# Optimization experiments

Measured on AMD Instinct MI355X. Metric: run time of the kernel, lower is better.

The kernel has to match this reference:

```python
import jax, jax.numpy as jnp
import numpy as np
import math

N_EMBD = 1024
N_HEAD = 16
HEAD_DIM = N_EMBD // N_HEAD

def setup_inputs() -> dict:
    key = jax.random.key(0)
    ks = jax.random.split(key, 9)
    B, T, C = 2, 2048, N_EMBD
    s = 1.0 / math.sqrt(C)
    return {
        "x": jax.random.normal(ks[0], (B, T, C), dtype=jnp.float32),
        "Wq": jax.random.normal(ks[1], (C, C), dtype=jnp.float32) * s,
        "bq": jnp.zeros((C,), dtype=jnp.float32),
        "Wk": jax.random.normal(ks[2], (C, C), dtype=jnp.float32) * s,
        "bk": jnp.zeros((C,), dtype=jnp.float32),
        "Wv": jax.random.normal(ks[3], (C, C), dtype=jnp.float32) * s,
        "bv": jnp.zeros((C,), dtype=jnp.float32),
        "Wp": jax.random.normal(ks[4], (C, C), dtype=jnp.float32) * s,
        "bp": jnp.zeros((C,), dtype=jnp.float32),
    }

def reference(x, Wq, bq, Wk, bk, Wv, bv, Wp, bp):
    B, T, C = x.shape
    H, D = N_HEAD, HEAD_DIM
    q = (x @ Wq + bq).reshape(B, T, H, D).transpose(0, 2, 1, 3)  # [B,H,T,D]
    k = (x @ Wk + bk).reshape(B, T, H, D).transpose(0, 2, 1, 3)
    v = (x @ Wv + bv).reshape(B, T, H, D).transpose(0, 2, 1, 3)
    att = jnp.einsum('bhqd,bhkd->bhqk', q, k) / math.sqrt(D)
    causal = jnp.tril(jnp.ones((T, T), dtype=bool))
    att = jnp.where(causal, att, -jnp.inf)
    att = jax.nn.softmax(att, axis=-1)
    att = jnp.nan_to_num(att)
    y = jnp.einsum('bhqk,bhkd->bhqd', att, v)
    y = y.transpose(0, 2, 1, 3).reshape(B, T, C)
    return y @ Wp + bp
```

## Files before the change

### kernel.cpp

```cpp
#include <hip/hip_runtime.h>
#include <hip/hip_bf16.h>
#include <stdint.h>

typedef unsigned short u16;
typedef __attribute__((ext_vector_type(8))) short short8;
typedef __attribute__((ext_vector_type(4))) float f32x4;

static __device__ __forceinline__ u16 f2bf(float f) {
  unsigned u = __builtin_bit_cast(unsigned, f);
  u += 0x7fffu + ((u >> 16) & 1u);
  return (u16)(u >> 16);
}

static __device__ __forceinline__ unsigned cvtpk(float lo, float hi) {
  unsigned r;
  asm("v_cvt_pk_bf16_f32 %0, %1, %2" : "=v"(r) : "v"(lo), "v"(hi));
  return r;
}

static __device__ __forceinline__ void gload16(const u16* g, u16* l) {
  __builtin_amdgcn_global_load_lds(
      (__attribute__((address_space(1))) void*)const_cast<u16*>(g),
      (__attribute__((address_space(3))) void*)l, 16, 0, 0);
}

__global__ __launch_bounds__(256) void prep_kernel(
    const float* __restrict__ x, const float* __restrict__ Wq,
    const float* __restrict__ Wk, const float* __restrict__ Wv,
    const float* __restrict__ Wp, u16* __restrict__ xb, u16* __restrict__ wt) {
  __shared__ float tile[64][65];
  int b = blockIdx.x;
  if (b < 2048) {
    size_t i = (size_t)b * 256 + threadIdx.x;
    const float4* xp = (const float4*)x + i * 2;
    float4 a = xp[0], v = xp[1];
    union { u16 u[8]; int4 q; } r;
    r.u[0] = f2bf(a.x); r.u[1] = f2bf(a.y); r.u[2] = f2bf(a.z); r.u[3] = f2bf(a.w);
    r.u[4] = f2bf(v.x); r.u[5] = f2bf(v.y); r.u[6] = f2bf(v.z); r.u[7] = f2bf(v.w);
    *(int4*)(xb + i * 8) = r.q;
  } else {
    int wb = b - 2048;
    int wz = wb >> 8, r8 = wb & 255;
    const float* W = (wz == 0) ? Wq : (wz == 1) ? Wk : (wz == 2) ? Wv : Wp;
    int n0 = (r8 & 15) * 64, k0 = (r8 >> 4) * 64;
    int tx = threadIdx.x & 63, ty = threadIdx.x >> 6;
#pragma unroll
    for (int r = 0; r < 16; ++r)
      tile[ty + 4 * r][tx] = W[(size_t)(k0 + ty + 4 * r) * 1024 + n0 + tx];
    __syncthreads();
    u16* dst = wt + (size_t)wz * 1024 * 1024;
#pragma unroll
    for (int r = 0; r < 16; ++r) {
      int n = ty + 4 * r;
      dst[(size_t)(n0 + n) * 1024 + k0 + tx] = f2bf(tile[tx][n]);
    }
  }
}

__global__ __launch_bounds__(256, 2) void gemm_qkv_kernel(
    const u16* __restrict__ A, const u16* __restrict__ Bt, int Kdim,
    int GM, int GN, int RM, int RN,
    u16* __restrict__ qd, u16* __restrict__ kd, u16* __restrict__ vd,
    const float* __restrict__ bq, const float* __restrict__ bk,
    const float* __restrict__ bv) {
  __shared__ u16 Alds[8192];
  __shared__ u16 Blds[8192];
  int tid = threadIdx.x;
  int lane = tid & 63, w = tid >> 6;
  int l15 = lane & 15, lg = lane >> 4;
  int flat = blockIdx.x;
  int xcd = flat & 7, idx = flat >> 3;
  int rnc = GN / RN;
  int rm = (xcd / rnc) * RM, rn = (xcd % rnc) * RN;
  int im = idx % RM, in_ = idx / RM;
  int m0 = (rm + im) * 128, n0 = (rn + in_) * 128;
  int wm = (w >> 1) * 64, wn = (w & 1) * 64;
  int srow = lane >> 3;
  int colsw = ((lane & 7) * 8) ^ ((srow & 7) * 8);

  const u16* pA[4];
  const u16* pB[4];
  int dls[4];
#pragma unroll
  for (int j = 0; j < 4; ++j) {
    int issue = w * 4 + j;
    int row = issue * 8 + srow;
    pA[j] = A + (size_t)(m0 + row) * Kdim + colsw;
    pB[j] = Bt + (size_t)(n0 + row) * Kdim + colsw;
    dls[j] = issue * 512;
  }
  int kx = (l15 & 7) << 4;
  int ofs0 = (lg * 16) ^ kx, ofs1 = (64 + lg * 16) ^ kx;
  int rbA = (wm + l15) * 128, rbB = (wn + l15) * 128;

  f32x4 acc[4][4] = {};
  for (int kt = 0; kt < Kdim; kt += 64) {
#pragma unroll
    for (int j = 0; j < 4; ++j) {
      gload16(pA[j], Alds + dls[j]);
      gload16(pB[j], Blds + dls[j]);
      pA[j] += 64; pB[j] += 64;
    }
    __syncthreads();
    __builtin_amdgcn_s_setprio(1);
#pragma unroll
    for (int kk = 0; kk < 2; ++kk) {
      int o_ = kk ? ofs1 : ofs0;
      short8 a[4], b[4];
#pragma unroll
      for (int mt = 0; mt < 4; ++mt)
        a[mt] = *(const short8*)((const char*)Alds + (rbA + o_) + mt * 2048);
#pragma unroll
      for (int nt = 0; nt < 4; ++nt)
        b[nt] = *(const short8*)((const char*)Blds + (rbB + o_) + nt * 2048);
#pragma unroll
      for (int mt = 0; mt < 4; ++mt)
#pragma unroll
        for (int nt = 0; nt < 4; ++nt)
          acc[mt][nt] = __builtin_amdgcn_mfma_f32_16x16x32_bf16(a[mt], b[nt],
                                                                acc[mt][nt], 0, 0, 0);
    }
    __builtin_amdgcn_s_setprio(0);
    __syncthreads();
  }
#pragma unroll
  for (int nt = 0; nt < 4; ++nt) {
    int n = n0 + wn + nt * 16 + l15;
    int wi = n >> 10, nn = n & 1023, h = nn >> 6, d = nn & 63;
    const float* bb = (wi == 0) ? bq : (wi == 1) ? bk : bv;
    float bval = bb[nn];
    if (wi == 2) {
#pragma unroll
      for (int mt = 0; mt < 4; ++mt) {
        int m = m0 + wm + mt * 16 + lg * 4;
        int mb = m >> 11, t = m & 2047;
        unsigned lo = cvtpk(acc[mt][nt][0] + bval, acc[mt][nt][1] + bval);
        unsigned hi = cvtpk(acc[mt][nt][2] + bval, acc[mt][nt][3] + bval);
        *(uint2*)&vd[((size_t)(mb * 16 + h) * 64 + d) * 2048 + t] =
            make_uint2(lo, hi);
      }
    } else {
      u16* dst = (wi == 0) ? qd : kd;
#pragma unroll
      for (int mt = 0; mt < 4; ++mt) {
#pragma unroll
        for (int i = 0; i < 4; ++i) {
          int m = m0 + wm + mt * 16 + lg * 4 + i;
          int mb = m >> 11, t = m & 2047;
          dst[((size_t)(mb * 16 + h) * 2048 + t) * 64 + d] =
              f2bf(acc[mt][nt][i] + bval);
        }
      }
    }
  }
}

__global__ __launch_bounds__(256, 2) void gemm_proj_kernel(
    const u16* __restrict__ A, const u16* __restrict__ Bt,
    float* __restrict__ outf, const float* __restrict__ bias1) {
  __shared__ u16 Alds[2 * 8192];
  __shared__ u16 Blds[2 * 4096];
  int tid = threadIdx.x;
  int lane = tid & 63, w = tid >> 6;
  int l15 = lane & 15, lg = lane >> 4;
  int flat = blockIdx.x;
  int xcd = flat & 7, idx = flat >> 3;
  int rm = (xcd >> 1) * 8, rn = (xcd & 1) * 8;
  int m0 = (rm + (idx & 7)) * 128, n0 = (rn + (idx >> 3)) * 64;
  int wm = (w >> 1) * 64, wn = (w & 1) * 32;
  int srow = lane >> 3;
  int colsw = ((lane & 7) * 8) ^ ((srow & 7) * 8);

  const u16* pA[4];
  int dlsA[4];
#pragma unroll
  for (int j = 0; j < 4; ++j) {
    int issue = w * 4 + j;
    int row = issue * 8 + srow;
    pA[j] = A + (size_t)(m0 + row) * 1024 + colsw;
    dlsA[j] = issue * 512;
  }
  const u16* pB[2];
  int dlsB[2];
#pragma unroll
  for (int it = 0; it < 2; ++it) {
    int chunk = it * 256 + tid;
    int row = chunk >> 3;
    int col = ((chunk & 7) * 8) ^ ((row & 7) * 8);
    pB[it] = Bt + (size_t)(n0 + row) * 1024 + col;
    dlsB[it] = (it * 256 + w * 64) * 8;
  }
  int kx = (l15 & 7) << 4;
  int ofs0 = (lg * 16) ^ kx, ofs1 = (64 + lg * 16) ^ kx;
  int rbA = (wm + l15) * 128, rbB = (wn + l15) * 128;

  auto stage = [&](int buf) {
    u16* Ad = Alds + buf * 8192;
    u16* Bd = Blds + buf * 4096;
#pragma unroll
    for (int j = 0; j < 4; ++j) { gload16(pA[j], Ad + dlsA[j]); pA[j] += 64; }
#pragma unroll
    for (int it = 0; it < 2; ++it) { gload16(pB[it], Bd + dlsB[it]); pB[it] += 64; }
  };

  f32x4 acc[4][2] = {};
  stage(0);
  int cur = 0;
  for (int kt = 0; kt < 1024; kt += 64) {
    __syncthreads();
    if (kt + 64 < 1024) stage(cur ^ 1);
    const char* Al = (const char*)Alds + cur * 16384;
    const char* Bl = (const char*)Blds + cur * 8192;
    __builtin_amdgcn_s_setprio(1);
#pragma unroll
    for (int kk = 0; kk < 2; ++kk) {
      int o_ = kk ? ofs1 : ofs0;
      short8 a[4], b[2];
#pragma unroll
      for (int mt = 0; mt < 4; ++mt)
        a[mt] = *(const short8*)(Al + (rbA + o_) + mt * 2048);
#pragma unroll
      for (int nt = 0; nt < 2; ++nt)
        b[nt] = *(const short8*)(Bl + (rbB + o_) + nt * 2048);
#pragma unroll
      for (int mt = 0; mt < 4; ++mt)
#pragma unroll
        for (int nt = 0; nt < 2; ++nt)
          acc[mt][nt] = __builtin_amdgcn_mfma_f32_16x16x32_bf16(a[mt], b[nt],
                                                                acc[mt][nt], 0, 0, 0);
    }
    __builtin_amdgcn_s_setprio(0);
    cur ^= 1;
  }
#pragma unroll
  for (int nt = 0; nt < 2; ++nt) {
    int n = n0 + wn + nt * 16 + l15;
    float bval = bias1[n];
#pragma unroll
    for (int mt = 0; mt < 4; ++mt) {
#pragma unroll
      for (int i = 0; i < 4; ++i) {
        int m = m0 + wm + mt * 16 + lg * 4 + i;
        outf[(size_t)m * 1024 + n] = acc[mt][nt][i] + bval;
      }
    }
  }
}

__global__ __launch_bounds__(256, 4) void fattn_kernel(const u16* __restrict__ qb,
                                                       const u16* __restrict__ kb,
                                                       const u16* __restrict__ vt,
                                                       u16* __restrict__ y) {
  __shared__ u16 Klds[4096];
  __shared__ u16 Vlds[4096];
  __shared__ u16 Plds[4096];
  int tid = threadIdx.x, lane = tid & 63, w = tid >> 6;
  int l15 = lane & 15, lg = lane >> 4;
  int flat = blockIdx.x;
  int bh = flat & 31;
  int g = flat >> 5;
  int qt;
  switch (g >> 3) {
    case 0:  qt = 31 - g; break;
    case 1:  qt = g - 8;  break;
    case 2:  qt = 39 - g; break;
    default: qt = g - 16; break;
  }
  size_t base = (size_t)bh * 2048 * 64;
  int mb = bh >> 4, h = bh & 15;
  const float SC = 0.125f * 1.44269504088896340736f;
  const float NINF = -__builtin_inff();

  int r0 = tid >> 3, c0 = ((tid & 7) * 8) ^ ((r0 & 7) << 3);
  int r1 = (256 + tid) >> 3, c1 = ((tid & 7) * 8) ^ ((r1 & 7) << 3);
  const u16* pK0 = kb + base + (size_t)r0 * 64 + c0;
  const u16* pK1 = kb + base + (size_t)r1 * 64 + c1;
  const u16* pV0 = vt + base + (size_t)r0 * 2048 + c0;
  const u16* pV1 = vt + base + (size_t)r1 * 2048 + c1;
  int dk0 = w * 512, dk1 = (256 + w * 64) * 8;
  int kx = (l15 & 7) << 4;
  int rb0 = l15 * 128 + ((lg * 16) ^ kx);
  int rb1 = l15 * 128 + ((64 + lg * 16) ^ kx);
  char* pbase = (char*)Plds + w * 2048;
  int pw0 = l15 * 128 + ((lg * 8) ^ kx);
  int pw1 = l15 * 128 + ((32 + lg * 8) ^ kx);
  int pw2 = l15 * 128 + ((64 + lg * 8) ^ kx);
  int pw3 = l15 * 128 + ((96 + lg * 8) ^ kx);

  int qw = qt * 64 + w * 16;
  int qr = qw + l15;
  short8 qf[2];
#pragma unroll
  for (int kk = 0; kk < 2; ++kk)
    qf[kk] = *(const short8*)&qb[base + (size_t)qr * 64 + kk * 32 + lg * 8];
  f32x4 o[4] = {};
  float mrow = NINF, lrow = 0.f;
  int ntiles = qt + 1;
  for (int j = 0; j < ntiles; ++j) {
    gload16(pK0, Klds + dk0); gload16(pK1, Klds + dk1);
    gload16(pV0, Vlds + dk0); gload16(pV1, Vlds + dk1);
    pK0 += 4096; pK1 += 4096; pV0 += 64; pV1 += 64;
    __syncthreads();
    f32x4 s[4] = {};
    __builtin_amdgcn_s_setprio(1);
#pragma unroll
    for (int kk = 0; kk < 2; ++kk) {
      int o_ = kk ? rb1 : rb0;
      short8 ka[4];
#pragma unroll
      for (int nt = 0; nt < 4; ++nt)
        ka[nt] = *(const short8*)((const char*)Klds + o_ + nt * 2048);
#pragma unroll
      for (int nt = 0; nt < 4; ++nt)
        s[nt] = __builtin_amdgcn_mfma_f32_16x16x32_bf16(ka[nt], qf[kk], s[nt], 0, 0, 0);
    }
    __builtin_amdgcn_s_setprio(0);
    float rs[16];
    if (j == qt) {
      int k0 = j * 64;
#pragma unroll
      for (int nt = 0; nt < 4; ++nt)
#pragma unroll
        for (int i = 0; i < 4; ++i) {
          int ka_ = k0 + nt * 16 + lg * 4 + i;
          rs[nt * 4 + i] = (ka_ > qr) ? NINF : s[nt][i];
        }
    } else {
#pragma unroll
      for (int nt = 0; nt < 4; ++nt)
#pragma unroll
        for (int i = 0; i < 4; ++i) rs[nt * 4 + i] = s[nt][i];
    }
    float rmax = fmaxf(
        fmaxf(fmaxf(fmaxf(rs[0], rs[1]), fmaxf(rs[2], rs[3])),
              fmaxf(fmaxf(rs[4], rs[5]), fmaxf(rs[6], rs[7]))),
        fmaxf(fmaxf(fmaxf(rs[8], rs[9]), fmaxf(rs[10], rs[11])),
              fmaxf(fmaxf(rs[12], rs[13]), fmaxf(rs[14], rs[15]))));
    float tmax = rmax * SC;
    if (!__all(tmax <= mrow + 8.f)) {
      float t2 = fmaxf(tmax, __shfl_xor(tmax, 16));
      t2 = fmaxf(t2, __shfl_xor(t2, 32));
      float vmax = fmaxf(t2, mrow);
      float scale = exp2f(mrow - vmax);
      mrow = vmax;
      lrow *= scale;
#pragma unroll
      for (int dn = 0; dn < 4; ++dn) o[dn] *= scale;
    }
    float p[16];
#pragma unroll
    for (int u = 0; u < 16; ++u) p[u] = exp2f(fmaf(rs[u], SC, -mrow));
    float pr0 = ((p[0] + p[1]) + (p[2] + p[3])) + ((p[4] + p[5]) + (p[6] + p[7]));
    float pr1 = ((p[8] + p[9]) + (p[10] + p[11])) + ((p[12] + p[13]) + (p[14] + p[15]));
    lrow += pr0 + pr1;
    *(uint2*)(pbase + pw0) = make_uint2(cvtpk(p[0], p[1]), cvtpk(p[2], p[3]));
    *(uint2*)(pbase + pw1) = make_uint2(cvtpk(p[4], p[5]), cvtpk(p[6], p[7]));
    *(uint2*)(pbase + pw2) = make_uint2(cvtpk(p[8], p[9]), cvtpk(p[10], p[11]));
    *(uint2*)(pbase + pw3) = make_uint2(cvtpk(p[12], p[13]), cvtpk(p[14], p[15]));
    __builtin_amdgcn_s_setprio(1);
#pragma unroll
    for (int kk = 0; kk < 2; ++kk) {
      int o_ = kk ? rb1 : rb0;
      short8 ap = *(const short8*)(pbase + o_);
#pragma unroll
      for (int dn = 0; dn < 4; ++dn) {
        short8 bv_ = *(const short8*)((const char*)Vlds + o_ + dn * 2048);
        o[dn] = __builtin_amdgcn_mfma_f32_16x16x32_bf16(bv_, ap, o[dn], 0, 0, 0);
      }
    }
    __builtin_amdgcn_s_setprio(0);
    __syncthreads();
  }
  lrow += __shfl_xor(lrow, 16);
  lrow += __shfl_xor(lrow, 32);
  float inv = 1.f / lrow;
  size_t rb = ((size_t)(mb * 2048 + qr)) * 1024 + (size_t)h * 64;
#pragma unroll
  for (int dn = 0; dn < 4; ++dn) {
    unsigned lo = cvtpk(o[dn][0] * inv, o[dn][1] * inv);
    unsigned hi = cvtpk(o[dn][2] * inv, o[dn][3] * inv);
    *(uint2*)&y[rb + dn * 16 + lg * 4] = make_uint2(lo, hi);
  }
}

extern "C" void kernel_launch(void* const* d_in, const int* in_sizes, int n_in,
                              void* d_out, int out_size, void* d_ws, size_t ws_size,
                              hipStream_t stream) {
  const float* x  = (const float*)d_in[0];
  const float* Wq = (const float*)d_in[1];
  const float* bq = (const float*)d_in[2];
  const float* Wk = (const float*)d_in[3];
  const float* bk = (const float*)d_in[4];
  const float* Wv = (const float*)d_in[5];
  const float* bv = (const float*)d_in[6];
  const float* Wp = (const float*)d_in[7];
  const float* bp = (const float*)d_in[8];
  float* out = (float*)d_out;
  char* ws = (char*)d_ws;
  u16* xb   = (u16*)(ws);
  u16* wt   = (u16*)(ws + ((size_t)8 << 20));
  u16* qbuf = (u16*)(ws + ((size_t)16 << 20));
  u16* kbuf = (u16*)(ws + ((size_t)24 << 20));
  u16* vtb  = (u16*)(ws + ((size_t)32 << 20));
  u16* ybuf = (u16*)(ws + ((size_t)40 << 20));

  prep_kernel<<<dim3(3072), dim3(256), 0, stream>>>(x, Wq, Wk, Wv, Wp, xb, wt);
  gemm_qkv_kernel<<<dim3(768), dim3(256), 0, stream>>>(
      xb, wt, 1024, 32, 24, 8, 12, qbuf, kbuf, vtb, bq, bk, bv);
  fattn_kernel<<<dim3(1024), dim3(256), 0, stream>>>(qbuf, kbuf, vtb, ybuf);
  gemm_proj_kernel<<<dim3(512), dim3(256), 0, stream>>>(
      ybuf, wt + (size_t)3 * 1024 * 1024, out, bp);
  (void)in_sizes; (void)n_in; (void)out_size; (void)ws_size;
}
```

Before: 101.5 us.

## Split causal attention KV range into paired halves and merge with combine kernel

Each attention block now processes two partial query tiles: the first half of the KV range for tile u and the second half for tile 31-u. This evens out the causal-triangle work per block, which previously ranged from 1 to 32 KV tiles. Each half writes unnormalized bf16 output plus its per-row (max, sum) statistics. A new combine kernel then rescales and merges the two halves into the final y. The cost is an extra kernel launch, extra global traffic for the partial outputs and statistics, and an extra bf16 rounding of the partial outputs. The partial buffers reuse workspace regions whose earlier contents (x and the Q/K/V weights) have already been consumed.

```diff
diff --git a/kernel.cpp b/kernel.cpp
--- a/kernel.cpp
+++ b/kernel.cpp
@@ -10,6 +10,11 @@
   unsigned u = __builtin_bit_cast(unsigned, f);
   u += 0x7fffu + ((u >> 16) & 1u);
   return (u16)(u >> 16);
+}
+
+static __device__ __forceinline__ float bf2f(u16 v) {
+  unsigned u = (unsigned)v << 16;
+  return __builtin_bit_cast(float, u);
 }
 
 static __device__ __forceinline__ unsigned cvtpk(float lo, float hi) {
@@ -247,10 +252,10 @@
   }
 }
 
-__global__ __launch_bounds__(256, 4) void fattn_kernel(const u16* __restrict__ qb,
-                                                       const u16* __restrict__ kb,
-                                                       const u16* __restrict__ vt,
-                                                       u16* __restrict__ y) {
+__global__ __launch_bounds__(256, 4) void fattn_kernel(
+    const u16* __restrict__ qb, const u16* __restrict__ kb,
+    const u16* __restrict__ vt, u16* __restrict__ y,
+    u16* __restrict__ poA, float2* __restrict__ mlA, float2* __restrict__ mlB) {
   __shared__ u16 Klds[4096];
   __shared__ u16 Vlds[4096];
   __shared__ u16 Plds[4096];
@@ -258,14 +263,7 @@
   int l15 = lane & 15, lg = lane >> 4;
   int flat = blockIdx.x;
   int bh = flat & 31;
-  int g = flat >> 5;
-  int qt;
-  switch (g >> 3) {
-    case 0:  qt = 31 - g; break;
-    case 1:  qt = g - 8;  break;
-    case 2:  qt = 39 - g; break;
-    default: qt = g - 16; break;
-  }
+  int u = flat >> 5;
   size_t base = (size_t)bh * 2048 * 64;
   int mb = bh >> 4, h = bh & 15;
   const float SC = 0.125f * 1.44269504088896340736f;
@@ -273,10 +271,6 @@
 
   int r0 = tid >> 3, c0 = ((tid & 7) * 8) ^ ((r0 & 7) << 3);
   int r1 = (256 + tid) >> 3, c1 = ((tid & 7) * 8) ^ ((r1 & 7) << 3);
-  const u16* pK0 = kb + base + (size_t)r0 * 64 + c0;
-  const u16* pK1 = kb + base + (size_t)r1 * 64 + c1;
-  const u16* pV0 = vt + base + (size_t)r0 * 2048 + c0;
-  const u16* pV1 = vt + base + (size_t)r1 * 2048 + c1;
   int dk0 = w * 512, dk1 = (256 + w * 64) * 8;
   int kx = (l15 & 7) << 4;
   int rb0 = l15 * 128 + ((lg * 16) ^ kx);
@@ -287,100 +281,136 @@
   int pw2 = l15 * 128 + ((64 + lg * 8) ^ kx);
   int pw3 = l15 * 128 + ((96 + lg * 8) ^ kx);
 
-  int qw = qt * 64 + w * 16;
-  int qr = qw + l15;
-  short8 qf[2];
-#pragma unroll
-  for (int kk = 0; kk < 2; ++kk)
-    qf[kk] = *(const short8*)&qb[base + (size_t)qr * 64 + kk * 32 + lg * 8];
-  f32x4 o[4] = {};
-  float mrow = NINF, lrow = 0.f;
-  int ntiles = qt + 1;
-  for (int j = 0; j < ntiles; ++j) {
-    gload16(pK0, Klds + dk0); gload16(pK1, Klds + dk1);
-    gload16(pV0, Vlds + dk0); gload16(pV1, Vlds + dk1);
-    pK0 += 4096; pK1 += 4096; pV0 += 64; pV1 += 64;
-    __syncthreads();
-    f32x4 s[4] = {};
-    __builtin_amdgcn_s_setprio(1);
-#pragma unroll
-    for (int kk = 0; kk < 2; ++kk) {
-      int o_ = kk ? rb1 : rb0;
-      short8 ka[4];
-#pragma unroll
-      for (int nt = 0; nt < 4; ++nt)
-        ka[nt] = *(const short8*)((const char*)Klds + o_ + nt * 2048);
-#pragma unroll
-      for (int nt = 0; nt < 4; ++nt)
-        s[nt] = __builtin_amdgcn_mfma_f32_16x16x32_bf16(ka[nt], qf[kk], s[nt], 0, 0, 0);
-    }
-    __builtin_amdgcn_s_setprio(0);
-    float rs[16];
-    if (j == qt) {
-      int k0 = j * 64;
-#pragma unroll
-      for (int nt = 0; nt < 4; ++nt)
-#pragma unroll
-        for (int i = 0; i < 4; ++i) {
-          int ka_ = k0 + nt * 16 + lg * 4 + i;
-          rs[nt * 4 + i] = (ka_ > qr) ? NINF : s[nt][i];
+  for (int pc = 0; pc < 2; ++pc) {
+    int qt = pc ? (31 - u) : u;
+    int sp = (qt + 2) >> 1;
+    int j0 = pc ? sp : 0;
+    int j1 = pc ? (qt + 1) : sp;
+    int qw = qt * 64 + w * 16;
+    int qr = qw + l15;
+    short8 qf[2];
+#pragma unroll
+    for (int kk = 0; kk < 2; ++kk)
+      qf[kk] = *(const short8*)&qb[base + (size_t)qr * 64 + kk * 32 + lg * 8];
+    f32x4 o[4] = {};
+    float mrow = NINF, lrow = 0.f;
+    const u16* pK0 = kb + base + (size_t)(j0 * 64 + r0) * 64 + c0;
+    const u16* pK1 = kb + base + (size_t)(j0 * 64 + r1) * 64 + c1;
+    const u16* pV0 = vt + base + (size_t)r0 * 2048 + j0 * 64 + c0;
+    const u16* pV1 = vt + base + (size_t)r1 * 2048 + j0 * 64 + c1;
+    for (int j = j0; j < j1; ++j) {
+      gload16(pK0, Klds + dk0); gload16(pK1, Klds + dk1);
+      gload16(pV0, Vlds + dk0); gload16(pV1, Vlds + dk1);
+      pK0 += 4096; pK1 += 4096; pV0 += 64; pV1 += 64;
+      __syncthreads();
+      f32x4 s[4] = {};
+      __builtin_amdgcn_s_setprio(1);
+#pragma unroll
+      for (int kk = 0; kk < 2; ++kk) {
+        int o_ = kk ? rb1 : rb0;
+        short8 ka[4];
+#pragma unroll
+        for (int nt = 0; nt < 4; ++nt)
+          ka[nt] = *(const short8*)((const char*)Klds + o_ + nt * 2048);
+#pragma unroll
+        for (int nt = 0; nt < 4; ++nt)
+          s[nt] = __builtin_amdgcn_mfma_f32_16x16x32_bf16(ka[nt], qf[kk], s[nt], 0, 0, 0);
+      }
+      __builtin_amdgcn_s_setprio(0);
+      float rs[16];
+      if (j == qt) {
+        int k0 = j * 64;
+#pragma unroll
+        for (int nt = 0; nt < 4; ++nt)
+#pragma unroll
+          for (int i = 0; i < 4; ++i) {
+            int ka_ = k0 + nt * 16 + lg * 4 + i;
+            rs[nt * 4 + i] = (ka_ > qr) ? NINF : s[nt][i];
+          }
+      } else {
+#pragma unroll
+        for (int nt = 0; nt < 4; ++nt)
+#pragma unroll
+          for (int i = 0; i < 4; ++i) rs[nt * 4 + i] = s[nt][i];
+      }
+      float rmax = fmaxf(
+          fmaxf(fmaxf(fmaxf(rs[0], rs[1]), fmaxf(rs[2], rs[3])),
+                fmaxf(fmaxf(rs[4], rs[5]), fmaxf(rs[6], rs[7]))),
+          fmaxf(fmaxf(fmaxf(rs[8], rs[9]), fmaxf(rs[10], rs[11])),
+                fmaxf(fmaxf(rs[12], rs[13]), fmaxf(rs[14], rs[15]))));
+      float tmax = rmax * SC;
+      if (!__all(tmax <= mrow + 8.f)) {
+        float t2 = fmaxf(tmax, __shfl_xor(tmax, 16));
+        t2 = fmaxf(t2, __shfl_xor(t2, 32));
+        float vmax = fmaxf(t2, mrow);
+        float scale = exp2f(mrow - vmax);
+        mrow = vmax;
+        lrow *= scale;
+#pragma unroll
+        for (int dn = 0; dn < 4; ++dn) o[dn] *= scale;
+      }
+      float p[16];
+#pragma unroll
+      for (int u2 = 0; u2 < 16; ++u2) p[u2] = exp2f(fmaf(rs[u2], SC, -mrow));
+      float pr0 = ((p[0] + p[1]) + (p[2] + p[3])) + ((p[4] + p[5]) + (p[6] + p[7]));
+      float pr1 = ((p[8] + p[9]) + (p[10] + p[11])) + ((p[12] + p[13]) + (p[14] + p[15]));
+      lrow += pr0 + pr1;
+      *(uint2*)(pbase + pw0) = make_uint2(cvtpk(p[0], p[1]), cvtpk(p[2], p[3]));
+      *(uint2*)(pbase + pw1) = make_uint2(cvtpk(p[4], p[5]), cvtpk(p[6], p[7]));
+      *(uint2*)(pbase + pw2) = make_uint2(cvtpk(p[8], p[9]), cvtpk(p[10], p[11]));
+      *(uint2*)(pbase + pw3) = make_uint2(cvtpk(p[12], p[13]), cvtpk(p[14], p[15]));
+      __builtin_amdgcn_s_setprio(1);
+#pragma unroll
+      for (int kk = 0; kk < 2; ++kk) {
+        int o_ = kk ? rb1 : rb0;
+        short8 ap = *(const short8*)(pbase + o_);
+#pragma unroll
+        for (int dn = 0; dn < 4; ++dn) {
+          short8 bv_ = *(const short8*)((const char*)Vlds + o_ + dn * 2048);
+          o[dn] = __builtin_amdgcn_mfma_f32_16x16x32_bf16(bv_, ap, o[dn], 0, 0, 0);
         }
-    } else {
-#pragma unroll
-      for (int nt = 0; nt < 4; ++nt)
-#pragma unroll
-        for (int i = 0; i < 4; ++i) rs[nt * 4 + i] = s[nt][i];
-    }
-    float rmax = fmaxf(
-        fmaxf(fmaxf(fmaxf(rs[0], rs[1]), fmaxf(rs[2], rs[3])),
-              fmaxf(fmaxf(rs[4], rs[5]), fmaxf(rs[6], rs[7]))),
-        fmaxf(fmaxf(fmaxf(rs[8], rs[9]), fmaxf(rs[10], rs[11])),
-              fmaxf(fmaxf(rs[12], rs[13]), fmaxf(rs[14], rs[15]))));
-    float tmax = rmax * SC;
-    if (!__all(tmax <= mrow + 8.f)) {
-      float t2 = fmaxf(tmax, __shfl_xor(tmax, 16));
-      t2 = fmaxf(t2, __shfl_xor(t2, 32));
-      float vmax = fmaxf(t2, mrow);
-      float scale = exp2f(mrow - vmax);
-      mrow = vmax;
-      lrow *= scale;
-#pragma unroll
-      for (int dn = 0; dn < 4; ++dn) o[dn] *= scale;
-    }
-    float p[16];
-#pragma unroll
-    for (int u = 0; u < 16; ++u) p[u] = exp2f(fmaf(rs[u], SC, -mrow));
-    float pr0 = ((p[0] + p[1]) + (p[2] + p[3])) + ((p[4] + p[5]) + (p[6] + p[7]));
-    float pr1 = ((p[8] + p[9]) + (p[10] + p[11])) + ((p[12] + p[13]) + (p[14] + p[15]));
-    lrow += pr0 + pr1;
-    *(uint2*)(pbase + pw0) = make_uint2(cvtpk(p[0], p[1]), cvtpk(p[2], p[3]));
-    *(uint2*)(pbase + pw1) = make_uint2(cvtpk(p[4], p[5]), cvtpk(p[6], p[7]));
-    *(uint2*)(pbase + pw2) = make_uint2(cvtpk(p[8], p[9]), cvtpk(p[10], p[11]));
-    *(uint2*)(pbase + pw3) = make_uint2(cvtpk(p[12], p[13]), cvtpk(p[14], p[15]));
-    __builtin_amdgcn_s_setprio(1);
-#pragma unroll
-    for (int kk = 0; kk < 2; ++kk) {
-      int o_ = kk ? rb1 : rb0;
-      short8 ap = *(const short8*)(pbase + o_);
-#pragma unroll
-      for (int dn = 0; dn < 4; ++dn) {
-        short8 bv_ = *(const short8*)((const char*)Vlds + o_ + dn * 2048);
-        o[dn] = __builtin_amdgcn_mfma_f32_16x16x32_bf16(bv_, ap, o[dn], 0, 0, 0);
-      }
-    }
-    __builtin_amdgcn_s_setprio(0);
-    __syncthreads();
-  }
-  lrow += __shfl_xor(lrow, 16);
-  lrow += __shfl_xor(lrow, 32);
-  float inv = 1.f / lrow;
-  size_t rb = ((size_t)(mb * 2048 + qr)) * 1024 + (size_t)h * 64;
-#pragma unroll
-  for (int dn = 0; dn < 4; ++dn) {
-    unsigned lo = cvtpk(o[dn][0] * inv, o[dn][1] * inv);
-    unsigned hi = cvtpk(o[dn][2] * inv, o[dn][3] * inv);
-    *(uint2*)&y[rb + dn * 16 + lg * 4] = make_uint2(lo, hi);
-  }
+      }
+      __builtin_amdgcn_s_setprio(0);
+      __syncthreads();
+    }
+    lrow += __shfl_xor(lrow, 16);
+    lrow += __shfl_xor(lrow, 32);
+    size_t rb = ((size_t)(mb * 2048 + qr)) * 1024 + (size_t)h * 64;
+    u16* dst = pc ? y : poA;
+#pragma unroll
+    for (int dn = 0; dn < 4; ++dn) {
+      unsigned lo = cvtpk(o[dn][0], o[dn][1]);
+      unsigned hi = cvtpk(o[dn][2], o[dn][3]);
+      *(uint2*)&dst[rb + dn * 16 + lg * 4] = make_uint2(lo, hi);
+    }
+    if (lg == 0)
+      (pc ? mlB : mlA)[bh * 2048 + qr] = make_float2(mrow, lrow);
+  }
+}
+
+__global__ __launch_bounds__(256) void combine_kernel(
+    const u16* __restrict__ poA, const float2* __restrict__ mlA,
+    const float2* __restrict__ mlB, u16* __restrict__ y) {
+  int idx = blockIdx.x * 256 + threadIdx.x;
+  int pos = idx * 4;
+  int row = pos >> 10;
+  int hq = (pos >> 6) & 15;
+  int qr = row & 2047, mb2 = row >> 11;
+  int rid = (mb2 * 16 + hq) * 2048 + qr;
+  float2 a = mlA[rid], b = mlB[rid];
+  float m = fmaxf(a.x, b.x);
+  float ea = exp2f(a.x - m), eb = exp2f(b.x - m);
+  float inv = 1.f / (a.y * ea + b.y * eb);
+  ea *= inv; eb *= inv;
+  uint2 pa = *(const uint2*)&poA[pos];
+  uint2 pb = *(const uint2*)&y[pos];
+  const u16* au = (const u16*)&pa;
+  const u16* bu = (const u16*)&pb;
+  float v0 = bf2f(au[0]) * ea + bf2f(bu[0]) * eb;
+  float v1 = bf2f(au[1]) * ea + bf2f(bu[1]) * eb;
+  float v2 = bf2f(au[2]) * ea + bf2f(bu[2]) * eb;
+  float v3 = bf2f(au[3]) * ea + bf2f(bu[3]) * eb;
+  *(uint2*)&y[pos] = make_uint2(cvtpk(v0, v1), cvtpk(v2, v3));
 }
 
 extern "C" void kernel_launch(void* const* d_in, const int* in_sizes, int n_in,
@@ -403,11 +433,16 @@
   u16* kbuf = (u16*)(ws + ((size_t)24 << 20));
   u16* vtb  = (u16*)(ws + ((size_t)32 << 20));
   u16* ybuf = (u16*)(ws + ((size_t)40 << 20));
+  u16*    poA = (u16*)(ws);
+  float2* mlA = (float2*)(ws + ((size_t)8 << 20));
+  float2* mlB = (float2*)(ws + ((size_t)8 << 20) + (512 << 10));
 
   prep_kernel<<<dim3(3072), dim3(256), 0, stream>>>(x, Wq, Wk, Wv, Wp, xb, wt);
   gemm_qkv_kernel<<<dim3(768), dim3(256), 0, stream>>>(
       xb, wt, 1024, 32, 24, 8, 12, qbuf, kbuf, vtb, bq, bk, bv);
-  fattn_kernel<<<dim3(1024), dim3(256), 0, stream>>>(qbuf, kbuf, vtb, ybuf);
+  fattn_kernel<<<dim3(1024), dim3(256), 0, stream>>>(qbuf, kbuf, vtb, ybuf,
+                                                     poA, mlA, mlB);
+  combine_kernel<<<dim3(4096), dim3(256), 0, stream>>>(poA, mlA, mlB, ybuf);
   gemm_proj_kernel<<<dim3(512), dim3(256), 0, stream>>>(
       ybuf, wt + (size_t)3 * 1024 * 1024, out, bp);
   (void)in_sizes; (void)n_in; (void)out_size; (void)ws_size;
```

Result: slower. 110.4 us (+8.7%).

## Process 128-key K/V tiles per iteration in causal flash attention

Applied to the files above, without the earlier changes.

Doubles the K/V tile per loop iteration from 64 to 128 keys, doubling the K and V LDS buffers and updating the load addressing and swizzle for the wider V rows. This halves the number of barriers, global-to-LDS load rounds and online-softmax max/rescale checks per query tile. P·V is done in two 64-key halves that reuse the per-wave P buffer. The cost is more LDS per block, which could limit occupancy, plus wasted compute on a fully masked half tile at the diagonal when the query tile index is even.

```diff
diff --git a/kernel.cpp b/kernel.cpp
--- a/kernel.cpp
+++ b/kernel.cpp
@@ -251,8 +251,8 @@
                                                        const u16* __restrict__ kb,
                                                        const u16* __restrict__ vt,
                                                        u16* __restrict__ y) {
-  __shared__ u16 Klds[4096];
-  __shared__ u16 Vlds[4096];
+  __shared__ u16 Klds[8192];
+  __shared__ u16 Vlds[8192];
   __shared__ u16 Plds[4096];
   int tid = threadIdx.x, lane = tid & 63, w = tid >> 6;
   int l15 = lane & 15, lg = lane >> 4;
@@ -271,16 +271,22 @@
   const float SC = 0.125f * 1.44269504088896340736f;
   const float NINF = -__builtin_inff();
 
-  int r0 = tid >> 3, c0 = ((tid & 7) * 8) ^ ((r0 & 7) << 3);
-  int r1 = (256 + tid) >> 3, c1 = ((tid & 7) * 8) ^ ((r1 & 7) << 3);
-  const u16* pK0 = kb + base + (size_t)r0 * 64 + c0;
-  const u16* pK1 = kb + base + (size_t)r1 * 64 + c1;
-  const u16* pV0 = vt + base + (size_t)r0 * 2048 + c0;
-  const u16* pV1 = vt + base + (size_t)r1 * 2048 + c1;
-  int dk0 = w * 512, dk1 = (256 + w * 64) * 8;
+  const u16* pK[4];
+  const u16* pV[4];
+  int dls[4];
+#pragma unroll
+  for (int it = 0; it < 4; ++it) {
+    int c = it * 256 + tid;
+    int rK = c >> 3, cK = ((c & 7) * 8) ^ ((rK & 7) << 3);
+    pK[it] = kb + base + (size_t)rK * 64 + cK;
+    int dV = c >> 4, cV = ((c & 15) * 8) ^ ((dV & 7) << 3);
+    pV[it] = vt + base + (size_t)dV * 2048 + cV;
+    dls[it] = (it * 256 + w * 64) * 8;
+  }
   int kx = (l15 & 7) << 4;
-  int rb0 = l15 * 128 + ((lg * 16) ^ kx);
-  int rb1 = l15 * 128 + ((64 + lg * 16) ^ kx);
+  int ofs0 = (lg * 16) ^ kx, ofs1 = (64 + lg * 16) ^ kx;
+  int rb0 = l15 * 128 + ofs0, rb1 = l15 * 128 + ofs1;
+  int vb0 = l15 * 256 + ofs0, vb1 = l15 * 256 + ofs1;
   char* pbase = (char*)Plds + w * 2048;
   int pw0 = l15 * 128 + ((lg * 8) ^ kx);
   int pw1 = l15 * 128 + ((32 + lg * 8) ^ kx);
@@ -289,19 +295,23 @@
 
   int qw = qt * 64 + w * 16;
   int qr = qw + l15;
+  int jdiag = qt >> 1;
   short8 qf[2];
 #pragma unroll
   for (int kk = 0; kk < 2; ++kk)
     qf[kk] = *(const short8*)&qb[base + (size_t)qr * 64 + kk * 32 + lg * 8];
   f32x4 o[4] = {};
   float mrow = NINF, lrow = 0.f;
-  int ntiles = qt + 1;
-  for (int j = 0; j < ntiles; ++j) {
-    gload16(pK0, Klds + dk0); gload16(pK1, Klds + dk1);
-    gload16(pV0, Vlds + dk0); gload16(pV1, Vlds + dk1);
-    pK0 += 4096; pK1 += 4096; pV0 += 64; pV1 += 64;
-    __syncthreads();
-    f32x4 s[4] = {};
+  int ntiles = (qt + 2) >> 1;
+  for (int jj = 0; jj < ntiles; ++jj) {
+#pragma unroll
+    for (int it = 0; it < 4; ++it) {
+      gload16(pK[it], Klds + dls[it]);
+      gload16(pV[it], Vlds + dls[it]);
+      pK[it] += 8192; pV[it] += 128;
+    }
+    __syncthreads();
+    f32x4 s0[4] = {}, s1[4] = {};
     __builtin_amdgcn_s_setprio(1);
 #pragma unroll
     for (int kk = 0; kk < 2; ++kk) {
@@ -312,30 +322,48 @@
         ka[nt] = *(const short8*)((const char*)Klds + o_ + nt * 2048);
 #pragma unroll
       for (int nt = 0; nt < 4; ++nt)
-        s[nt] = __builtin_amdgcn_mfma_f32_16x16x32_bf16(ka[nt], qf[kk], s[nt], 0, 0, 0);
+        s0[nt] = __builtin_amdgcn_mfma_f32_16x16x32_bf16(ka[nt], qf[kk], s0[nt], 0, 0, 0);
+    }
+#pragma unroll
+    for (int kk = 0; kk < 2; ++kk) {
+      int o_ = 8192 + (kk ? rb1 : rb0);
+      short8 ka[4];
+#pragma unroll
+      for (int nt = 0; nt < 4; ++nt)
+        ka[nt] = *(const short8*)((const char*)Klds + o_ + nt * 2048);
+#pragma unroll
+      for (int nt = 0; nt < 4; ++nt)
+        s1[nt] = __builtin_amdgcn_mfma_f32_16x16x32_bf16(ka[nt], qf[kk], s1[nt], 0, 0, 0);
     }
     __builtin_amdgcn_s_setprio(0);
-    float rs[16];
-    if (j == qt) {
-      int k0 = j * 64;
-#pragma unroll
-      for (int nt = 0; nt < 4; ++nt)
-#pragma unroll
-        for (int i = 0; i < 4; ++i) {
-          int ka_ = k0 + nt * 16 + lg * 4 + i;
-          rs[nt * 4 + i] = (ka_ > qr) ? NINF : s[nt][i];
-        }
-    } else {
-#pragma unroll
-      for (int nt = 0; nt < 4; ++nt)
-#pragma unroll
-        for (int i = 0; i < 4; ++i) rs[nt * 4 + i] = s[nt][i];
-    }
-    float rmax = fmaxf(
-        fmaxf(fmaxf(fmaxf(rs[0], rs[1]), fmaxf(rs[2], rs[3])),
-              fmaxf(fmaxf(rs[4], rs[5]), fmaxf(rs[6], rs[7]))),
-        fmaxf(fmaxf(fmaxf(rs[8], rs[9]), fmaxf(rs[10], rs[11])),
-              fmaxf(fmaxf(rs[12], rs[13]), fmaxf(rs[14], rs[15]))));
+    float rs[32];
+#pragma unroll
+    for (int nt = 0; nt < 4; ++nt)
+#pragma unroll
+      for (int i = 0; i < 4; ++i) {
+        rs[nt * 4 + i] = s0[nt][i];
+        rs[16 + nt * 4 + i] = s1[nt][i];
+      }
+    if (jj == jdiag) {
+      int k0 = jj * 128;
+#pragma unroll
+      for (int hh = 0; hh < 2; ++hh)
+#pragma unroll
+        for (int nt = 0; nt < 4; ++nt)
+#pragma unroll
+          for (int i = 0; i < 4; ++i) {
+            int ka_ = k0 + hh * 64 + nt * 16 + lg * 4 + i;
+            if (ka_ > qr) rs[hh * 16 + nt * 4 + i] = NINF;
+          }
+    }
+    float t16[16];
+#pragma unroll
+    for (int u2 = 0; u2 < 16; ++u2) t16[u2] = fmaxf(rs[u2], rs[u2 + 16]);
+#pragma unroll
+    for (int u2 = 0; u2 < 8; ++u2) t16[u2] = fmaxf(t16[u2], t16[u2 + 8]);
+#pragma unroll
+    for (int u2 = 0; u2 < 4; ++u2) t16[u2] = fmaxf(t16[u2], t16[u2 + 4]);
+    float rmax = fmaxf(fmaxf(t16[0], t16[1]), fmaxf(t16[2], t16[3]));
     float tmax = rmax * SC;
     if (!__all(tmax <= mrow + 8.f)) {
       float t2 = fmaxf(tmax, __shfl_xor(tmax, 16));
@@ -347,28 +375,39 @@
 #pragma unroll
       for (int dn = 0; dn < 4; ++dn) o[dn] *= scale;
     }
-    float p[16];
-#pragma unroll
-    for (int u = 0; u < 16; ++u) p[u] = exp2f(fmaf(rs[u], SC, -mrow));
-    float pr0 = ((p[0] + p[1]) + (p[2] + p[3])) + ((p[4] + p[5]) + (p[6] + p[7]));
-    float pr1 = ((p[8] + p[9]) + (p[10] + p[11])) + ((p[12] + p[13]) + (p[14] + p[15]));
-    lrow += pr0 + pr1;
-    *(uint2*)(pbase + pw0) = make_uint2(cvtpk(p[0], p[1]), cvtpk(p[2], p[3]));
-    *(uint2*)(pbase + pw1) = make_uint2(cvtpk(p[4], p[5]), cvtpk(p[6], p[7]));
-    *(uint2*)(pbase + pw2) = make_uint2(cvtpk(p[8], p[9]), cvtpk(p[10], p[11]));
-    *(uint2*)(pbase + pw3) = make_uint2(cvtpk(p[12], p[13]), cvtpk(p[14], p[15]));
-    __builtin_amdgcn_s_setprio(1);
-#pragma unroll
-    for (int kk = 0; kk < 2; ++kk) {
-      int o_ = kk ? rb1 : rb0;
-      short8 ap = *(const short8*)(pbase + o_);
-#pragma unroll
-      for (int dn = 0; dn < 4; ++dn) {
-        short8 bv_ = *(const short8*)((const char*)Vlds + o_ + dn * 2048);
-        o[dn] = __builtin_amdgcn_mfma_f32_16x16x32_bf16(bv_, ap, o[dn], 0, 0, 0);
+#pragma unroll
+    for (int u2 = 0; u2 < 32; ++u2) rs[u2] = exp2f(fmaf(rs[u2], SC, -mrow));
+    {
+      float a0 = 0.f;
+#pragma unroll
+      for (int u2 = 0; u2 < 8; ++u2)
+        a0 += (rs[u2] + rs[u2 + 8]) + (rs[u2 + 16] + rs[u2 + 24]);
+      lrow += a0;
+    }
+#pragma unroll
+    for (int hh = 0; hh < 2; ++hh) {
+      int h16 = hh * 16;
+      *(uint2*)(pbase + pw0) = make_uint2(cvtpk(rs[h16 + 0], rs[h16 + 1]),
+                                          cvtpk(rs[h16 + 2], rs[h16 + 3]));
+      *(uint2*)(pbase + pw1) = make_uint2(cvtpk(rs[h16 + 4], rs[h16 + 5]),
+                                          cvtpk(rs[h16 + 6], rs[h16 + 7]));
+      *(uint2*)(pbase + pw2) = make_uint2(cvtpk(rs[h16 + 8], rs[h16 + 9]),
+                                          cvtpk(rs[h16 + 10], rs[h16 + 11]));
+      *(uint2*)(pbase + pw3) = make_uint2(cvtpk(rs[h16 + 12], rs[h16 + 13]),
+                                          cvtpk(rs[h16 + 14], rs[h16 + 15]));
+      __builtin_amdgcn_s_setprio(1);
+#pragma unroll
+      for (int kk = 0; kk < 2; ++kk) {
+        short8 ap = *(const short8*)(pbase + (kk ? rb1 : rb0));
+        int vo = hh * 128 + (kk ? vb1 : vb0);
+#pragma unroll
+        for (int dn = 0; dn < 4; ++dn) {
+          short8 bv_ = *(const short8*)((const char*)Vlds + vo + dn * 4096);
+          o[dn] = __builtin_amdgcn_mfma_f32_16x16x32_bf16(bv_, ap, o[dn], 0, 0, 0);
+        }
       }
-    }
-    __builtin_amdgcn_s_setprio(0);
+      __builtin_amdgcn_s_setprio(0);
+    }
     __syncthreads();
   }
   lrow += __shfl_xor(lrow, 16);
```

After: 101.8 us. Within noise of the previous version (+0.3%).

## Rewrite flash attention with 32x32 MFMA, 2-wave blocks and register P shuffle

Applied to the files above, without the earlier changes.

The attention kernel now uses 32x32x16 bf16 MFMA tiles, with each wave owning 32 query rows and blocks cut from four waves to two. The P matrix is no longer staged through LDS. Each lane packs its probabilities to bf16 and swaps halves with the partner lane via shfl_xor to build the B operand directly, which removes the P LDS buffer and its writes and reads. Row-max and sum reductions also need fewer cross-lane shuffles. The cost is more registers per thread, lower launch-bounds occupancy, and more global-to-LDS load work per thread for the K/V tiles.

```diff
diff --git a/kernel.cpp b/kernel.cpp
--- a/kernel.cpp
+++ b/kernel.cpp
@@ -5,6 +5,7 @@
 typedef unsigned short u16;
 typedef __attribute__((ext_vector_type(8))) short short8;
 typedef __attribute__((ext_vector_type(4))) float f32x4;
+typedef __attribute__((ext_vector_type(16))) float f32x16;
 
 static __device__ __forceinline__ u16 f2bf(float f) {
   unsigned u = __builtin_bit_cast(unsigned, f);
@@ -247,15 +248,14 @@
   }
 }
 
-__global__ __launch_bounds__(256, 4) void fattn_kernel(const u16* __restrict__ qb,
+__global__ __launch_bounds__(128, 2) void fattn_kernel(const u16* __restrict__ qb,
                                                        const u16* __restrict__ kb,
                                                        const u16* __restrict__ vt,
                                                        u16* __restrict__ y) {
   __shared__ u16 Klds[4096];
   __shared__ u16 Vlds[4096];
-  __shared__ u16 Plds[4096];
   int tid = threadIdx.x, lane = tid & 63, w = tid >> 6;
-  int l15 = lane & 15, lg = lane >> 4;
+  int l31 = lane & 31, hi = lane >> 5;
   int flat = blockIdx.x;
   int bh = flat & 31;
   int g = flat >> 5;
@@ -271,115 +271,132 @@
   const float SC = 0.125f * 1.44269504088896340736f;
   const float NINF = -__builtin_inff();
 
-  int r0 = tid >> 3, c0 = ((tid & 7) * 8) ^ ((r0 & 7) << 3);
-  int r1 = (256 + tid) >> 3, c1 = ((tid & 7) * 8) ^ ((r1 & 7) << 3);
-  const u16* pK0 = kb + base + (size_t)r0 * 64 + c0;
-  const u16* pK1 = kb + base + (size_t)r1 * 64 + c1;
-  const u16* pV0 = vt + base + (size_t)r0 * 2048 + c0;
-  const u16* pV1 = vt + base + (size_t)r1 * 2048 + c1;
-  int dk0 = w * 512, dk1 = (256 + w * 64) * 8;
-  int kx = (l15 & 7) << 4;
-  int rb0 = l15 * 128 + ((lg * 16) ^ kx);
-  int rb1 = l15 * 128 + ((64 + lg * 16) ^ kx);
-  char* pbase = (char*)Plds + w * 2048;
-  int pw0 = l15 * 128 + ((lg * 8) ^ kx);
-  int pw1 = l15 * 128 + ((32 + lg * 8) ^ kx);
-  int pw2 = l15 * 128 + ((64 + lg * 8) ^ kx);
-  int pw3 = l15 * 128 + ((96 + lg * 8) ^ kx);
-
-  int qw = qt * 64 + w * 16;
-  int qr = qw + l15;
-  short8 qf[2];
-#pragma unroll
-  for (int kk = 0; kk < 2; ++kk)
-    qf[kk] = *(const short8*)&qb[base + (size_t)qr * 64 + kk * 32 + lg * 8];
-  f32x4 o[4] = {};
+  const u16* pK[4];
+  const u16* pV[4];
+  int dls[4];
+#pragma unroll
+  for (int it = 0; it < 4; ++it) {
+    int c = it * 128 + tid;
+    int rr = c >> 3, cc = ((c & 7) * 8) ^ ((rr & 7) << 3);
+    pK[it] = kb + base + (size_t)rr * 64 + cc;
+    pV[it] = vt + base + (size_t)rr * 2048 + cc;
+    dls[it] = it * 1024 + w * 512;
+  }
+  int kx2 = (lane & 7) << 4;
+  int ofs[4];
+#pragma unroll
+  for (int c = 0; c < 4; ++c) ofs[c] = (c * 32 + hi * 16) ^ kx2;
+  int rowA = l31 * 128;
+
+  int qr = qt * 64 + w * 32 + l31;
+  short8 qf[4];
+#pragma unroll
+  for (int c = 0; c < 4; ++c)
+    qf[c] = *(const short8*)&qb[base + (size_t)qr * 64 + c * 16 + hi * 8];
+
+  f32x16 o0 = {}, o1 = {};
   float mrow = NINF, lrow = 0.f;
   int ntiles = qt + 1;
   for (int j = 0; j < ntiles; ++j) {
-    gload16(pK0, Klds + dk0); gload16(pK1, Klds + dk1);
-    gload16(pV0, Vlds + dk0); gload16(pV1, Vlds + dk1);
-    pK0 += 4096; pK1 += 4096; pV0 += 64; pV1 += 64;
-    __syncthreads();
-    f32x4 s[4] = {};
+#pragma unroll
+    for (int it = 0; it < 4; ++it) {
+      gload16(pK[it], Klds + dls[it]);
+      gload16(pV[it], Vlds + dls[it]);
+      pK[it] += 4096; pV[it] += 64;
+    }
+    __syncthreads();
+    f32x16 s0 = {}, s1 = {};
     __builtin_amdgcn_s_setprio(1);
 #pragma unroll
-    for (int kk = 0; kk < 2; ++kk) {
-      int o_ = kk ? rb1 : rb0;
-      short8 ka[4];
-#pragma unroll
-      for (int nt = 0; nt < 4; ++nt)
-        ka[nt] = *(const short8*)((const char*)Klds + o_ + nt * 2048);
-#pragma unroll
-      for (int nt = 0; nt < 4; ++nt)
-        s[nt] = __builtin_amdgcn_mfma_f32_16x16x32_bf16(ka[nt], qf[kk], s[nt], 0, 0, 0);
+    for (int c = 0; c < 4; ++c) {
+      short8 ka0 = *(const short8*)((const char*)Klds + rowA + ofs[c]);
+      short8 ka1 = *(const short8*)((const char*)Klds + 4096 + rowA + ofs[c]);
+      s0 = __builtin_amdgcn_mfma_f32_32x32x16_bf16(ka0, qf[c], s0, 0, 0, 0);
+      s1 = __builtin_amdgcn_mfma_f32_32x32x16_bf16(ka1, qf[c], s1, 0, 0, 0);
     }
     __builtin_amdgcn_s_setprio(0);
-    float rs[16];
+    float rs[32];
+#pragma unroll
+    for (int r = 0; r < 16; ++r) { rs[r] = s0[r]; rs[16 + r] = s1[r]; }
     if (j == qt) {
       int k0 = j * 64;
 #pragma unroll
-      for (int nt = 0; nt < 4; ++nt)
-#pragma unroll
-        for (int i = 0; i < 4; ++i) {
-          int ka_ = k0 + nt * 16 + lg * 4 + i;
-          rs[nt * 4 + i] = (ka_ > qr) ? NINF : s[nt][i];
+      for (int sub = 0; sub < 2; ++sub)
+#pragma unroll
+        for (int r = 0; r < 16; ++r) {
+          int kv = k0 + sub * 32 + (r & 3) + 8 * (r >> 2) + 4 * hi;
+          if (kv > qr) rs[sub * 16 + r] = NINF;
         }
-    } else {
-#pragma unroll
-      for (int nt = 0; nt < 4; ++nt)
-#pragma unroll
-        for (int i = 0; i < 4; ++i) rs[nt * 4 + i] = s[nt][i];
-    }
-    float rmax = fmaxf(
-        fmaxf(fmaxf(fmaxf(rs[0], rs[1]), fmaxf(rs[2], rs[3])),
-              fmaxf(fmaxf(rs[4], rs[5]), fmaxf(rs[6], rs[7]))),
-        fmaxf(fmaxf(fmaxf(rs[8], rs[9]), fmaxf(rs[10], rs[11])),
-              fmaxf(fmaxf(rs[12], rs[13]), fmaxf(rs[14], rs[15]))));
+    }
+    float t16[16];
+#pragma unroll
+    for (int u2 = 0; u2 < 16; ++u2) t16[u2] = fmaxf(rs[u2], rs[u2 + 16]);
+#pragma unroll
+    for (int u2 = 0; u2 < 8; ++u2) t16[u2] = fmaxf(t16[u2], t16[u2 + 8]);
+#pragma unroll
+    for (int u2 = 0; u2 < 4; ++u2) t16[u2] = fmaxf(t16[u2], t16[u2 + 4]);
+    float rmax = fmaxf(fmaxf(t16[0], t16[1]), fmaxf(t16[2], t16[3]));
     float tmax = rmax * SC;
     if (!__all(tmax <= mrow + 8.f)) {
-      float t2 = fmaxf(tmax, __shfl_xor(tmax, 16));
-      t2 = fmaxf(t2, __shfl_xor(t2, 32));
+      float t2 = fmaxf(tmax, __shfl_xor(tmax, 32));
       float vmax = fmaxf(t2, mrow);
       float scale = exp2f(mrow - vmax);
       mrow = vmax;
       lrow *= scale;
-#pragma unroll
-      for (int dn = 0; dn < 4; ++dn) o[dn] *= scale;
-    }
-    float p[16];
-#pragma unroll
-    for (int u = 0; u < 16; ++u) p[u] = exp2f(fmaf(rs[u], SC, -mrow));
-    float pr0 = ((p[0] + p[1]) + (p[2] + p[3])) + ((p[4] + p[5]) + (p[6] + p[7]));
-    float pr1 = ((p[8] + p[9]) + (p[10] + p[11])) + ((p[12] + p[13]) + (p[14] + p[15]));
-    lrow += pr0 + pr1;
-    *(uint2*)(pbase + pw0) = make_uint2(cvtpk(p[0], p[1]), cvtpk(p[2], p[3]));
-    *(uint2*)(pbase + pw1) = make_uint2(cvtpk(p[4], p[5]), cvtpk(p[6], p[7]));
-    *(uint2*)(pbase + pw2) = make_uint2(cvtpk(p[8], p[9]), cvtpk(p[10], p[11]));
-    *(uint2*)(pbase + pw3) = make_uint2(cvtpk(p[12], p[13]), cvtpk(p[14], p[15]));
+      o0 *= scale; o1 *= scale;
+    }
+#pragma unroll
+    for (int u2 = 0; u2 < 32; ++u2) rs[u2] = exp2f(fmaf(rs[u2], SC, -mrow));
+    {
+      float a0 = 0.f;
+#pragma unroll
+      for (int u2 = 0; u2 < 8; ++u2)
+        a0 += (rs[u2] + rs[u2 + 8]) + (rs[u2 + 16] + rs[u2 + 24]);
+      lrow += a0;
+    }
     __builtin_amdgcn_s_setprio(1);
 #pragma unroll
-    for (int kk = 0; kk < 2; ++kk) {
-      int o_ = kk ? rb1 : rb0;
-      short8 ap = *(const short8*)(pbase + o_);
-#pragma unroll
-      for (int dn = 0; dn < 4; ++dn) {
-        short8 bv_ = *(const short8*)((const char*)Vlds + o_ + dn * 2048);
-        o[dn] = __builtin_amdgcn_mfma_f32_16x16x32_bf16(bv_, ap, o[dn], 0, 0, 0);
-      }
+    for (int ks = 0; ks < 4; ++ks) {
+      const int s2 = ks >> 1, c2 = ks & 1;
+      const int pb = s2 * 16 + 8 * c2;
+      unsigned w0 = cvtpk(rs[pb + 0], rs[pb + 1]);
+      unsigned w1 = cvtpk(rs[pb + 2], rs[pb + 3]);
+      unsigned w2 = cvtpk(rs[pb + 4], rs[pb + 5]);
+      unsigned w3 = cvtpk(rs[pb + 6], rs[pb + 7]);
+      unsigned e0 = (unsigned)__shfl_xor((int)w0, 32);
+      unsigned e1 = (unsigned)__shfl_xor((int)w1, 32);
+      unsigned e2 = (unsigned)__shfl_xor((int)w2, 32);
+      unsigned e3 = (unsigned)__shfl_xor((int)w3, 32);
+      uint4 fw;
+      fw.x = hi ? e2 : w0;
+      fw.y = hi ? e3 : w1;
+      fw.z = hi ? w2 : e0;
+      fw.w = hi ? w3 : e1;
+      short8 pf = __builtin_bit_cast(short8, fw);
+      short8 va0 = *(const short8*)((const char*)Vlds + rowA + ofs[ks]);
+      short8 va1 = *(const short8*)((const char*)Vlds + 4096 + rowA + ofs[ks]);
+      o0 = __builtin_amdgcn_mfma_f32_32x32x16_bf16(va0, pf, o0, 0, 0, 0);
+      o1 = __builtin_amdgcn_mfma_f32_32x32x16_bf16(va1, pf, o1, 0, 0, 0);
     }
     __builtin_amdgcn_s_setprio(0);
     __syncthreads();
   }
-  lrow += __shfl_xor(lrow, 16);
   lrow += __shfl_xor(lrow, 32);
   float inv = 1.f / lrow;
   size_t rb = ((size_t)(mb * 2048 + qr)) * 1024 + (size_t)h * 64;
 #pragma unroll
-  for (int dn = 0; dn < 4; ++dn) {
-    unsigned lo = cvtpk(o[dn][0] * inv, o[dn][1] * inv);
-    unsigned hi = cvtpk(o[dn][2] * inv, o[dn][3] * inv);
-    *(uint2*)&y[rb + dn * 16 + lg * 4] = make_uint2(lo, hi);
+  for (int gq = 0; gq < 4; ++gq) {
+    int d = 8 * gq + 4 * hi;
+    unsigned lo = cvtpk(o0[4 * gq + 0] * inv, o0[4 * gq + 1] * inv);
+    unsigned hi2 = cvtpk(o0[4 * gq + 2] * inv, o0[4 * gq + 3] * inv);
+    *(uint2*)&y[rb + d] = make_uint2(lo, hi2);
+  }
+#pragma unroll
+  for (int gq = 0; gq < 4; ++gq) {
+    int d = 32 + 8 * gq + 4 * hi;
+    unsigned lo = cvtpk(o1[4 * gq + 0] * inv, o1[4 * gq + 1] * inv);
+    unsigned hi2 = cvtpk(o1[4 * gq + 2] * inv, o1[4 * gq + 3] * inv);
+    *(uint2*)&y[rb + d] = make_uint2(lo, hi2);
   }
 }
 
@@ -407,7 +424,7 @@
   prep_kernel<<<dim3(3072), dim3(256), 0, stream>>>(x, Wq, Wk, Wv, Wp, xb, wt);
   gemm_qkv_kernel<<<dim3(768), dim3(256), 0, stream>>>(
       xb, wt, 1024, 32, 24, 8, 12, qbuf, kbuf, vtb, bq, bk, bv);
-  fattn_kernel<<<dim3(1024), dim3(256), 0, stream>>>(qbuf, kbuf, vtb, ybuf);
+  fattn_kernel<<<dim3(1024), dim3(128), 0, stream>>>(qbuf, kbuf, vtb, ybuf);
   gemm_proj_kernel<<<dim3(512), dim3(256), 0, stream>>>(
       ybuf, wt + (size_t)3 * 1024 * 1024, out, bp);
   (void)in_sizes; (void)n_in; (void)out_size; (void)ws_size;
```

After: 117.7 us. 16.0% more time.
